# Performance work log

Measured on AMD Instinct MI355X. Metric: run time of the kernel, lower is better.

The kernel has to match this reference:

```python
import jax, jax.numpy as jnp
import numpy as np

EPS = 1e-08


def setup_inputs() -> dict:
    key = jax.random.key(0)
    k_x, k_w1, k_b1, k_w2, k_b2 = jax.random.split(key, 5)
    B, C, T = 64, 64, 4000
    x = jax.random.normal(k_x, (B, C, T, 1), dtype=jnp.float32)
    # 1x1 Conv2D with in_channels=1, out_channels=8 -> weight is an 8-vector + bias
    w1 = jax.random.normal(k_w1, (8,), dtype=jnp.float32) * 0.5
    b1 = jax.random.normal(k_b1, (8,), dtype=jnp.float32) * 0.1
    w2 = jax.random.normal(k_w2, (8,), dtype=jnp.float32) * 0.5
    b2 = jax.random.normal(k_b2, (8,), dtype=jnp.float32) * 0.1
    # gamma is initialized to 0 in the module (residual identity at init);
    # use a nonzero value so the attention path is exercised numerically.
    gamma = jnp.float32(0.5)
    return {"x": x, "w1": w1, "b1": b1, "w2": w2, "b2": b2, "gamma": gamma}


def reference(x, w1, b1, w2, b2, gamma):
    B, C, T, _ = x.shape  # (B, num_ch, T, 1)
    # 1x1 conv with C_in=1: broadcast multiply-add, then flatten (T, 8) -> T*8
    q = (x * w1 + b1).reshape(B, C, T * 8)  # proj_query (B, C, T*8)
    k = (x * w2 + b2).reshape(B, C, T * 8)  # proj_key   (B, C, T*8)
    # energy = Q @ K^T  -> (B, C, C)
    energy = jnp.einsum('bcd,bed->bce', q, k)
    # custom min-max normalization along last axis, then softmax
    max_h = jnp.max(energy, axis=2, keepdims=True)
    min_h = jnp.min(energy, axis=2, keepdims=True)
    energy = (energy - min_h) / (max_h - min_h + EPS)
    attention = jax.nn.softmax(energy, axis=-1)
    xs = x[..., 0]  # squeeze last dim -> (B, C, T)
    # attention^T @ xs  (transpose_a=True)
    attended = jnp.einsum('bec,bet->bct', attention, xs)
    return gamma * attended[..., None] + x
```

## Files before the change

kernel.cpp:

```cpp
#include <hip/hip_runtime.h>

#define BB 64
#define CC 64
#define TT 4000

#define SLABS 16
#define TSLAB 250
#define GP_PITCH 264

#define TPB 128
#define NT2 ((TT + TPB - 1) / TPB)

#define GPART_ELEMS ((size_t)SLABS * BB * CC * CC)
#define SPART_ELEMS ((size_t)SLABS * BB * CC)
#define ATT_ELEMS   ((size_t)BB * CC * CC)

typedef short short8 __attribute__((ext_vector_type(8)));
typedef float f32x16 __attribute__((ext_vector_type(16)));

__device__ __forceinline__ short f2bf(float f) {
    unsigned u = __float_as_uint(f);
    u = (u + 0x7FFFu + ((u >> 16) & 1u)) >> 16;
    return (short)u;
}

__global__ __launch_bounds__(256)
void gram_mfma(const float* __restrict__ x, float* __restrict__ G_part,
               float* __restrict__ S_part) {
    __shared__ short xs[CC * GP_PITCH];
    __shared__ float sred[4 * 64];
    const int b    = blockIdx.x / SLABS;
    const int slab = blockIdx.x % SLABS;
    const int t0   = slab * TSLAB;
    const int tid  = threadIdx.x;
    const int lane = tid & 63;
    const int wave = tid >> 6;
    const float* xb = x + (size_t)b * CC * TT;

    for (int i = tid; i < 64 * 64; i += 256) {
        int row = i >> 6, tq = i & 63;
        float4 v = make_float4(0.f, 0.f, 0.f, 0.f);
        if (tq < 62) {
            v = *(const float4*)(xb + row * TT + t0 + 4 * tq);
        } else if (tq == 62) {
            const float* p = xb + row * TT + t0 + 248;
            v.x = p[0]; v.y = p[1];
        }
        short4 sv;
        sv.x = f2bf(v.x); sv.y = f2bf(v.y); sv.z = f2bf(v.z); sv.w = f2bf(v.w);
        *(short4*)(xs + row * GP_PITCH + 4 * tq) = sv;
    }
    __syncthreads();

    {
        const short* base = xs + lane * GP_PITCH + 64 * wave;
        float s = 0.f;
        #pragma unroll
        for (int j = 0; j < 8; ++j) {
            uint4 u = *(const uint4*)(base + 8 * j);
            s += __uint_as_float(u.x << 16) + __uint_as_float(u.x & 0xFFFF0000u);
            s += __uint_as_float(u.y << 16) + __uint_as_float(u.y & 0xFFFF0000u);
            s += __uint_as_float(u.z << 16) + __uint_as_float(u.z & 0xFFFF0000u);
            s += __uint_as_float(u.w << 16) + __uint_as_float(u.w & 0xFFFF0000u);
        }
        sred[wave * 64 + lane] = s;
    }
    __syncthreads();
    if (tid < 64) {
        float s = sred[tid] + sred[64 + tid] + sred[128 + tid] + sred[192 + tid];
        S_part[(slab * BB + b) * CC + tid] = s;
    }

    const int r0 = (wave >> 1) * 32, c0 = (wave & 1) * 32;
    const int m = lane & 31, half = lane >> 5;
    f32x16 acc;
    #pragma unroll
    for (int z = 0; z < 16; ++z) acc[z] = 0.f;
    #pragma unroll
    for (int ks = 0; ks < 16; ++ks) {
        const int k0 = ks * 16 + 8 * half;
        short8 av = *(const short8*)(xs + (r0 + m) * GP_PITCH + k0);
        short8 bv = *(const short8*)(xs + (c0 + m) * GP_PITCH + k0);
        acc = __builtin_amdgcn_mfma_f32_32x32x16_bf16(av, bv, acc, 0, 0, 0);
    }
    float* gp = G_part + ((size_t)slab * BB + b) * (CC * CC);
    #pragma unroll
    for (int r = 0; r < 16; ++r) {
        const int row = (r & 3) + 8 * (r >> 2) + 4 * half;
        gp[(r0 + row) * CC + (c0 + m)] = acc[r];
    }
}

__global__ __launch_bounds__(256)
void softmax_fused(const float* __restrict__ w1, const float* __restrict__ b1,
                   const float* __restrict__ w2, const float* __restrict__ b2,
                   const float* __restrict__ G_part, const float* __restrict__ S_part,
                   float* __restrict__ att) {
    __shared__ float Es[64 * 65];
    __shared__ float Sb[64];
    __shared__ float red_mn[4 * 64], red_mx[4 * 64], red_sm[4 * 64];
    const int b   = blockIdx.x;
    const int tid = threadIdx.x;
    const int c = tid & 63, q = tid >> 6;

    for (int j = tid; j < 4096; j += 256) {
        float s = 0.f;
        #pragma unroll
        for (int sl = 0; sl < SLABS; ++sl)
            s += G_part[((size_t)sl * BB + b) * 4096 + j];
        Es[(j >> 6) * 65 + (j & 63)] = s;
    }
    if (tid < 64) {
        float s = 0.f;
        #pragma unroll
        for (int sl = 0; sl < SLABS; ++sl)
            s += S_part[(sl * BB + b) * CC + tid];
        Sb[tid] = s;
    }
    float A = 0.f, Bc = 0.f, Be = 0.f, Cc = 0.f;
    #pragma unroll
    for (int j = 0; j < 8; ++j) {
        float a1 = w1[j], a2 = w2[j], q1 = b1[j], q2 = b2[j];
        A += a1 * a2; Bc += a1 * q2; Be += q1 * a2; Cc += q1 * q2;
    }
    Cc *= (float)TT;
    __syncthreads();

    const float sc = Sb[c];
    float ev[16], mn = 1e30f, mx = -1e30f;
    #pragma unroll
    for (int i = 0; i < 16; ++i) {
        const int e = 16 * q + i;
        float en = A * Es[c * 65 + e] + Bc * sc + Be * Sb[e] + Cc;
        ev[i] = en;
        mn = fminf(mn, en); mx = fmaxf(mx, en);
    }
    red_mn[q * 64 + c] = mn; red_mx[q * 64 + c] = mx;
    __syncthreads();
    mn = fminf(fminf(red_mn[c], red_mn[64 + c]), fminf(red_mn[128 + c], red_mn[192 + c]));
    mx = fmaxf(fmaxf(red_mx[c], red_mx[64 + c]), fmaxf(red_mx[128 + c], red_mx[192 + c]));
    const float ninv = 1.f / (mx - mn + 1e-8f);
    float pv[16], ls = 0.f;
    #pragma unroll
    for (int i = 0; i < 16; ++i) {
        float p = __expf((ev[i] - mn) * ninv);
        pv[i] = p; ls += p;
    }
    red_sm[q * 64 + c] = ls;
    __syncthreads();
    const float rinv = 1.f / (red_sm[c] + red_sm[64 + c] + red_sm[128 + c] + red_sm[192 + c]);
    #pragma unroll
    for (int i = 0; i < 16; ++i) Es[c * 65 + 16 * q + i] = pv[i] * rinv;
    __syncthreads();
    float* ab = att + (size_t)b * 4096;
    for (int j = tid; j < 4096; j += 256)
        ab[j] = Es[(j >> 6) * 65 + (j & 63)];
}

__global__ __launch_bounds__(256)
void apply_kernel(const float* __restrict__ x, const float* __restrict__ att,
                  const float* __restrict__ gamma, float* __restrict__ out) {
    __shared__ float As[CC * CC];
    __shared__ float xs[CC * TPB];
    const int b  = blockIdx.x / NT2;
    const int t0 = (blockIdx.x % NT2) * TPB;
    const int tid = threadIdx.x;
    const int tx = tid & 15, ty = tid >> 4;
    const float* attb = att + (size_t)b * CC * CC;
    const float* xb   = x + (size_t)b * CC * TT;

    for (int idx = tid; idx < CC * CC / 4; idx += 256)
        *(float4*)(As + 4 * idx) = *(const float4*)(attb + 4 * idx);
    for (int idx = tid; idx < CC * (TPB / 4); idx += 256) {
        int e = idx >> 5;
        int p = idx & 31;
        int t = t0 + 4 * p;
        float4 v = make_float4(0.f, 0.f, 0.f, 0.f);
        if (t < TT) v = *(const float4*)(xb + e * TT + t);
        *(float4*)(xs + e * TPB + 4 * p) = v;
    }
    __syncthreads();

    float acc[4][8];
    #pragma unroll
    for (int i = 0; i < 4; ++i)
        #pragma unroll
        for (int j = 0; j < 8; ++j) acc[i][j] = 0.f;

    for (int e = 0; e < CC; ++e) {
        float4 m  = *(const float4*)(As + e * CC + 4 * ty);
        float4 v1 = *(const float4*)(xs + e * TPB + 4 * tx);
        float4 v2 = *(const float4*)(xs + e * TPB + 64 + 4 * tx);
        #pragma unroll
        for (int i = 0; i < 4; ++i) {
            float mi = (i == 0) ? m.x : (i == 1) ? m.y : (i == 2) ? m.z : m.w;
            acc[i][0] += mi * v1.x; acc[i][1] += mi * v1.y;
            acc[i][2] += mi * v1.z; acc[i][3] += mi * v1.w;
            acc[i][4] += mi * v2.x; acc[i][5] += mi * v2.y;
            acc[i][6] += mi * v2.z; acc[i][7] += mi * v2.w;
        }
    }

    const float gm = gamma[0];
    float* ob = out + (size_t)b * CC * TT;
    #pragma unroll
    for (int i = 0; i < 4; ++i) {
        const int c = 4 * ty + i;
        const int t1 = t0 + 4 * tx;
        const int t2 = t0 + 64 + 4 * tx;
        if (t1 < TT) {
            float4 xr = *(const float4*)(xs + c * TPB + 4 * tx);
            float4 r = make_float4(gm * acc[i][0] + xr.x, gm * acc[i][1] + xr.y,
                                   gm * acc[i][2] + xr.z, gm * acc[i][3] + xr.w);
            *(float4*)(ob + c * TT + t1) = r;
        }
        if (t2 < TT) {
            float4 xr = *(const float4*)(xs + c * TPB + 64 + 4 * tx);
            float4 r = make_float4(gm * acc[i][4] + xr.x, gm * acc[i][5] + xr.y,
                                   gm * acc[i][6] + xr.z, gm * acc[i][7] + xr.w);
            *(float4*)(ob + c * TT + t2) = r;
        }
    }
}

extern "C" void kernel_launch(void* const* d_in, const int* in_sizes, int n_in,
                              void* d_out, int out_size, void* d_ws, size_t ws_size,
                              hipStream_t stream) {
    const float* x  = (const float*)d_in[0];
    const float* w1 = (const float*)d_in[1];
    const float* b1 = (const float*)d_in[2];
    const float* w2 = (const float*)d_in[3];
    const float* b2 = (const float*)d_in[4];
    const float* gm = (const float*)d_in[5];
    float* out = (float*)d_out;

    float* G_part = (float*)d_ws;
    float* S_part = G_part + GPART_ELEMS;
    float* att    = S_part + SPART_ELEMS;

    hipLaunchKernelGGL(gram_mfma, dim3(BB * SLABS), dim3(256), 0, stream,
                       x, G_part, S_part);
    hipLaunchKernelGGL(softmax_fused, dim3(BB), dim3(256), 0, stream,
                       w1, b1, w2, b2, G_part, S_part, att);
    hipLaunchKernelGGL(apply_kernel, dim3(BB * NT2), dim3(256), 0, stream,
                       x, att, gm, out);
}
```

Before: 169.3 us.

## Use bf16 MFMA in apply kernel and XOR-swizzle gram LDS layout

The apply stage's FP32 register-tiled FMA loop is replaced with bf16 32x32x16 MFMA instructions. Attention is written transposed so it can be loaded as the A operand, and x values are converted to bf16 on the fly from a padded LDS tile. The gram kernel's shared-memory layout gets an XOR swizzle on 16-byte chunks to cut bank conflicts on MFMA operand loads. The trade-off is lower precision in the attended product and strided scalar LDS reads with per-element conversion for the B operand.

New measurement: 167.2 us. About the same (-1.3%).

```diff
diff --git a/kernel.cpp b/kernel.cpp
--- a/kernel.cpp
+++ b/kernel.cpp
@@ -10,10 +10,11 @@
 
 #define TPB 128
 #define NT2 ((TT + TPB - 1) / TPB)
+#define XPITCH 132
+#define APITCH 72
 
 #define GPART_ELEMS ((size_t)SLABS * BB * CC * CC)
 #define SPART_ELEMS ((size_t)SLABS * BB * CC)
-#define ATT_ELEMS   ((size_t)BB * CC * CC)
 
 typedef short short8 __attribute__((ext_vector_type(8)));
 typedef float f32x16 __attribute__((ext_vector_type(16)));
@@ -22,6 +23,9 @@
     unsigned u = __float_as_uint(f);
     u = (u + 0x7FFFu + ((u >> 16) & 1u)) >> 16;
     return (short)u;
+}
+__device__ __forceinline__ float bfpair(unsigned u) {
+    return __uint_as_float(u << 16) + __uint_as_float(u & 0xFFFF0000u);
 }
 
 __global__ __launch_bounds__(256)
@@ -48,20 +52,20 @@
         }
         short4 sv;
         sv.x = f2bf(v.x); sv.y = f2bf(v.y); sv.z = f2bf(v.z); sv.w = f2bf(v.w);
-        *(short4*)(xs + row * GP_PITCH + 4 * tq) = sv;
+        int pc = (tq >> 1) ^ (row & 7);
+        *(short4*)(xs + row * GP_PITCH + pc * 8 + (tq & 1) * 4) = sv;
     }
     __syncthreads();
 
     {
-        const short* base = xs + lane * GP_PITCH + 64 * wave;
+        const short* rowp = xs + lane * GP_PITCH;
         float s = 0.f;
         #pragma unroll
         for (int j = 0; j < 8; ++j) {
-            uint4 u = *(const uint4*)(base + 8 * j);
-            s += __uint_as_float(u.x << 16) + __uint_as_float(u.x & 0xFFFF0000u);
-            s += __uint_as_float(u.y << 16) + __uint_as_float(u.y & 0xFFFF0000u);
-            s += __uint_as_float(u.z << 16) + __uint_as_float(u.z & 0xFFFF0000u);
-            s += __uint_as_float(u.w << 16) + __uint_as_float(u.w & 0xFFFF0000u);
+            int pc = (wave * 8 + j) ^ (lane & 7);
+            uint2 u0 = *(const uint2*)(rowp + pc * 8);
+            uint2 u1 = *(const uint2*)(rowp + pc * 8 + 4);
+            s += bfpair(u0.x) + bfpair(u0.y) + bfpair(u1.x) + bfpair(u1.y);
         }
         sred[wave * 64 + lane] = s;
     }
@@ -78,9 +82,9 @@
     for (int z = 0; z < 16; ++z) acc[z] = 0.f;
     #pragma unroll
     for (int ks = 0; ks < 16; ++ks) {
-        const int k0 = ks * 16 + 8 * half;
-        short8 av = *(const short8*)(xs + (r0 + m) * GP_PITCH + k0);
-        short8 bv = *(const short8*)(xs + (c0 + m) * GP_PITCH + k0);
+        const int ck = ks * 2 + half;
+        short8 av = *(const short8*)(xs + (r0 + m) * GP_PITCH + (ck ^ (m & 7)) * 8);
+        short8 bv = *(const short8*)(xs + (c0 + m) * GP_PITCH + (ck ^ (m & 7)) * 8);
         acc = __builtin_amdgcn_mfma_f32_32x32x16_bf16(av, bv, acc, 0, 0, 0);
     }
     float* gp = G_part + ((size_t)slab * BB + b) * (CC * CC);
@@ -95,7 +99,7 @@
 void softmax_fused(const float* __restrict__ w1, const float* __restrict__ b1,
                    const float* __restrict__ w2, const float* __restrict__ b2,
                    const float* __restrict__ G_part, const float* __restrict__ S_part,
-                   float* __restrict__ att) {
+                   float* __restrict__ attG) {
     __shared__ float Es[64 * 65];
     __shared__ float Sb[64];
     __shared__ float red_mn[4 * 64], red_mx[4 * 64], red_sm[4 * 64];
@@ -152,74 +156,72 @@
     #pragma unroll
     for (int i = 0; i < 16; ++i) Es[c * 65 + 16 * q + i] = pv[i] * rinv;
     __syncthreads();
-    float* ab = att + (size_t)b * 4096;
-    for (int j = tid; j < 4096; j += 256)
-        ab[j] = Es[(j >> 6) * 65 + (j & 63)];
+    float* ab = attG + (size_t)b * 4096;
+    for (int j = tid; j < 4096; j += 256) {
+        int cc = j >> 6, ee = j & 63;
+        ab[j] = Es[ee * 65 + cc];
+    }
 }
 
 __global__ __launch_bounds__(256)
-void apply_kernel(const float* __restrict__ x, const float* __restrict__ att,
-                  const float* __restrict__ gamma, float* __restrict__ out) {
-    __shared__ float As[CC * CC];
-    __shared__ float xs[CC * TPB];
+void apply_mfma(const float* __restrict__ x, const float* __restrict__ attG,
+                const float* __restrict__ gamma, float* __restrict__ out) {
+    __shared__ float xs[CC * XPITCH];
+    __shared__ short al[CC * APITCH];
     const int b  = blockIdx.x / NT2;
     const int t0 = (blockIdx.x % NT2) * TPB;
     const int tid = threadIdx.x;
-    const int tx = tid & 15, ty = tid >> 4;
-    const float* attb = att + (size_t)b * CC * CC;
-    const float* xb   = x + (size_t)b * CC * TT;
-
-    for (int idx = tid; idx < CC * CC / 4; idx += 256)
-        *(float4*)(As + 4 * idx) = *(const float4*)(attb + 4 * idx);
-    for (int idx = tid; idx < CC * (TPB / 4); idx += 256) {
-        int e = idx >> 5;
-        int p = idx & 31;
+    const int lane = tid & 63, wave = tid >> 6;
+    const float* xb = x + (size_t)b * CC * TT;
+    const float* ab = attG + (size_t)b * CC * CC;
+
+    for (int i = tid; i < CC * (TPB / 4); i += 256) {
+        int e = i >> 5, p = i & 31;
         int t = t0 + 4 * p;
         float4 v = make_float4(0.f, 0.f, 0.f, 0.f);
         if (t < TT) v = *(const float4*)(xb + e * TT + t);
-        *(float4*)(xs + e * TPB + 4 * p) = v;
-    }
-    __syncthreads();
-
-    float acc[4][8];
-    #pragma unroll
-    for (int i = 0; i < 4; ++i)
-        #pragma unroll
-        for (int j = 0; j < 8; ++j) acc[i][j] = 0.f;
-
-    for (int e = 0; e < CC; ++e) {
-        float4 m  = *(const float4*)(As + e * CC + 4 * ty);
-        float4 v1 = *(const float4*)(xs + e * TPB + 4 * tx);
-        float4 v2 = *(const float4*)(xs + e * TPB + 64 + 4 * tx);
-        #pragma unroll
-        for (int i = 0; i < 4; ++i) {
-            float mi = (i == 0) ? m.x : (i == 1) ? m.y : (i == 2) ? m.z : m.w;
-            acc[i][0] += mi * v1.x; acc[i][1] += mi * v1.y;
-            acc[i][2] += mi * v1.z; acc[i][3] += mi * v1.w;
-            acc[i][4] += mi * v2.x; acc[i][5] += mi * v2.y;
-            acc[i][6] += mi * v2.z; acc[i][7] += mi * v2.w;
+        *(float4*)(xs + e * XPITCH + 4 * p) = v;
+    }
+    for (int i = tid; i < CC * CC / 4; i += 256) {
+        int c = i >> 4, qq = i & 15;
+        float4 v = *(const float4*)(ab + c * CC + 4 * qq);
+        short4 sv;
+        sv.x = f2bf(v.x); sv.y = f2bf(v.y); sv.z = f2bf(v.z); sv.w = f2bf(v.w);
+        *(short4*)(al + c * APITCH + 4 * qq) = sv;
+    }
+    __syncthreads();
+
+    const int m = lane & 31, half = lane >> 5;
+    const int c0 = (wave & 1) * 32;
+    const int tb = (wave >> 1) * 64;
+    f32x16 acc0, acc1;
+    #pragma unroll
+    for (int z = 0; z < 16; ++z) { acc0[z] = 0.f; acc1[z] = 0.f; }
+
+    #pragma unroll
+    for (int ks = 0; ks < 4; ++ks) {
+        short8 av = *(const short8*)(al + (c0 + m) * APITCH + ks * 16 + 8 * half);
+        const int eb = ks * 16 + 8 * half;
+        short8 bv0, bv1;
+        #pragma unroll
+        for (int j = 0; j < 8; ++j) {
+            bv0[j] = f2bf(xs[(eb + j) * XPITCH + tb + m]);
+            bv1[j] = f2bf(xs[(eb + j) * XPITCH + tb + 32 + m]);
         }
+        acc0 = __builtin_amdgcn_mfma_f32_32x32x16_bf16(av, bv0, acc0, 0, 0, 0);
+        acc1 = __builtin_amdgcn_mfma_f32_32x32x16_bf16(av, bv1, acc1, 0, 0, 0);
     }
 
     const float gm = gamma[0];
     float* ob = out + (size_t)b * CC * TT;
     #pragma unroll
-    for (int i = 0; i < 4; ++i) {
-        const int c = 4 * ty + i;
-        const int t1 = t0 + 4 * tx;
-        const int t2 = t0 + 64 + 4 * tx;
-        if (t1 < TT) {
-            float4 xr = *(const float4*)(xs + c * TPB + 4 * tx);
-            float4 r = make_float4(gm * acc[i][0] + xr.x, gm * acc[i][1] + xr.y,
-                                   gm * acc[i][2] + xr.z, gm * acc[i][3] + xr.w);
-            *(float4*)(ob + c * TT + t1) = r;
-        }
-        if (t2 < TT) {
-            float4 xr = *(const float4*)(xs + c * TPB + 64 + 4 * tx);
-            float4 r = make_float4(gm * acc[i][4] + xr.x, gm * acc[i][5] + xr.y,
-                                   gm * acc[i][6] + xr.z, gm * acc[i][7] + xr.w);
-            *(float4*)(ob + c * TT + t2) = r;
-        }
+    for (int r = 0; r < 16; ++r) {
+        const int row = (r & 3) + 8 * (r >> 2) + 4 * half;
+        const int c = c0 + row;
+        const int tl0 = tb + m, tl1 = tb + 32 + m;
+        const int tg0 = t0 + tl0, tg1 = t0 + tl1;
+        if (tg0 < TT) ob[c * TT + tg0] = gm * acc0[r] + xs[c * XPITCH + tl0];
+        if (tg1 < TT) ob[c * TT + tg1] = gm * acc1[r] + xs[c * XPITCH + tl1];
     }
 }
 
@@ -236,12 +238,12 @@
 
     float* G_part = (float*)d_ws;
     float* S_part = G_part + GPART_ELEMS;
-    float* att    = S_part + SPART_ELEMS;
+    float* attG   = S_part + SPART_ELEMS;
 
     hipLaunchKernelGGL(gram_mfma, dim3(BB * SLABS), dim3(256), 0, stream,
                        x, G_part, S_part);
     hipLaunchKernelGGL(softmax_fused, dim3(BB), dim3(256), 0, stream,
-                       w1, b1, w2, b2, G_part, S_part, att);
-    hipLaunchKernelGGL(apply_kernel, dim3(BB * NT2), dim3(256), 0, stream,
-                       x, att, gm, out);
-}
+                       w1, b1, w2, b2, G_part, S_part, attG);
+    hipLaunchKernelGGL(apply_mfma, dim3(BB * NT2), dim3(256), 0, stream,
+                       x, attG, gm, out);
+}
```
